# Kernel tuning notes

Hardware: AMD Instinct MI355X
Metric: run time of the kernel (lower is better)

Reference implementation:

```python
import jax, jax.numpy as jnp
import numpy as np

B, L, D, N = 1, 4096, 1536, 12
d = D // N            # head_dim = 128
c = d // 2            # rope channels per head = 64
EPS = 1e-6
MAX_POS = 1024


def setup_inputs() -> dict:
    key = jax.random.key(0)
    ks = jax.random.split(key, 8)
    s = 0.02
    # RoPE tables: freqs[m, j] = m * theta^{-j/c}; torch stores exp(i*ang) as complex64
    inv = 1.0 / (10000.0 ** (jnp.arange(c, dtype=jnp.float32) / c))
    ang = jnp.arange(MAX_POS, dtype=jnp.float32)[:, None] * inv[None, :]
    return {
        'x': jax.random.normal(ks[0], (B, L, D), jnp.float32),
        'seq_lens': jnp.array([L], jnp.int32),
        'grid_sizes': jnp.array([[4, 32, 32]], jnp.int32),  # f*h*w == L
        'freqs_cos': jnp.cos(ang),
        'freqs_sin': jnp.sin(ang),
        'Wq': jax.random.normal(ks[1], (D, D), jnp.float32) * s,
        'bq': jnp.zeros((D,), jnp.float32),
        'Wk': jax.random.normal(ks[2], (D, D), jnp.float32) * s,
        'bk': jnp.zeros((D,), jnp.float32),
        'Wv': jax.random.normal(ks[3], (D, D), jnp.float32) * s,
        'bv': jnp.zeros((D,), jnp.float32),
        'Wo': jax.random.normal(ks[4], (D, D), jnp.float32) * s,
        'bo': jnp.zeros((D,), jnp.float32),
        'gq': jnp.ones((D,), jnp.float32),
        'gk': jnp.ones((D,), jnp.float32),
    }


def rms_norm(x, g):
    # WanRMSNorm over the full model dim, computed in fp32
    v = jnp.mean(x.astype(jnp.float32) ** 2, axis=-1, keepdims=True)
    return (x * jax.lax.rsqrt(v + EPS)).astype(x.dtype) * g


def rope_apply(x4, grid_sizes, fcos, fsin):
    # x4: [B, L, N, d]; grid_sizes: [B, 3]; applies 3D (f,h,w) RoPE per batch
    gs = np.asarray(grid_sizes)  # concrete grid sizes (structural constants)
    c1 = c - 2 * (c // 3)
    c2 = c // 3
    outs = []
    for i in range(x4.shape[0]):
        f, h, w = (int(gs[i, 0]), int(gs[i, 1]), int(gs[i, 2]))
        sl = f * h * w

        def grid(tab):
            a = jnp.broadcast_to(tab[:f, None, None, :c1], (f, h, w, c1))
            b = jnp.broadcast_to(tab[None, :h, None, c1:c1 + c2], (f, h, w, c2))
            cc = jnp.broadcast_to(tab[None, None, :w, c1 + c2:c], (f, h, w, c2))
            return jnp.concatenate([a, b, cc], axis=-1).reshape(sl, 1, c)

        cos_i, sin_i = grid(fcos), grid(fsin)
        xi = x4[i, :sl]                    # [sl, N, d]
        xr, xim = xi[..., 0::2], xi[..., 1::2]  # complex pairs are interleaved
        o_re = xr * cos_i - xim * sin_i
        o_im = xr * sin_i + xim * cos_i
        rot = jnp.stack([o_re, o_im], axis=-1).reshape(sl, x4.shape[2], d)
        outs.append(jnp.concatenate([rot, x4[i, sl:]], axis=0))
    return jnp.stack(outs).astype(x4.dtype)


def reference(x, seq_lens, grid_sizes, freqs_cos, freqs_sin,
              Wq, bq, Wk, bk, Wv, bv, Wo, bo, gq, gk):
    q = rms_norm(x @ Wq.T + bq, gq).reshape(B, L, N, d)
    k = rms_norm(x @ Wk.T + bk, gk).reshape(B, L, N, d)
    v = (x @ Wv.T + bv).reshape(B, L, N, d)
    q = rope_apply(q, grid_sizes, freqs_cos, freqs_sin)
    k = rope_apply(k, grid_sizes, freqs_cos, freqs_sin)
    scale = 1.0 / jnp.sqrt(jnp.float32(d))
    scores = jnp.einsum('bqnd,bknd->bnqk', q, k) * scale
    kmask = jnp.arange(L)[None, :] < seq_lens[:, None]        # [B, L]
    scores = jnp.where(kmask[:, None, None, :], scores, jnp.float32(-1e30))
    p = jax.nn.softmax(scores, axis=-1)
    out = jnp.einsum('bnqk,bknd->bqnd', p, v).reshape(B, L, D)
    return out @ Wo.T + bo
```

## Files before the change

### kernel.cpp

```cpp
#include <hip/hip_runtime.h>

#define L_ 4096
#define D_ 1536
#define NH 12
#define HD 128

typedef __attribute__((ext_vector_type(8))) __bf16 bf16x8;
typedef __attribute__((ext_vector_type(8))) unsigned short ushort8v;
typedef __attribute__((ext_vector_type(4))) float floatx4;

#if __has_builtin(__builtin_amdgcn_exp2f)
#define EXP2F(x) __builtin_amdgcn_exp2f(x)
#else
#define EXP2F(x) exp2f(x)
#endif

__device__ __forceinline__ unsigned short f2bf(float f) {
  union { float f; unsigned int u; } v; v.f = f;
  unsigned int u = v.u;
  return (unsigned short)((u + 0x7fffu + ((u >> 16) & 1u)) >> 16);
}
__device__ __forceinline__ float bf2f(unsigned short h) {
  union { unsigned int u; float f; } v; v.u = ((unsigned int)h) << 16;
  return v.f;
}

__global__ __launch_bounds__(256) void cvt_f32_bf16(const float* __restrict__ in,
                                                    unsigned short* __restrict__ out,
                                                    int n8) {
  int i = blockIdx.x * 256 + threadIdx.x;
  if (i >= n8) return;
  const float4* p = (const float4*)(in + (size_t)i * 8);
  float4 a = p[0], b = p[1];
  ushort8v o;
  o[0] = f2bf(a.x); o[1] = f2bf(a.y); o[2] = f2bf(a.z); o[3] = f2bf(a.w);
  o[4] = f2bf(b.x); o[5] = f2bf(b.y); o[6] = f2bf(b.z); o[7] = f2bf(b.w);
  *(ushort8v*)(out + (size_t)i * 8) = o;
}

template <int MODE>
__device__ __forceinline__ void gemm_core(const unsigned short* __restrict__ A,
                                          const unsigned short* __restrict__ Bw,
                                          const float* __restrict__ bias,
                                          void* __restrict__ Cout,
                                          int M, int Nn, int K,
                                          int m0, int n0,
                                          unsigned short* As, unsigned short* Bs) {
  int t = threadIdx.x;
  int lane = t & 63, wv = t >> 6;
  int wm = (wv & 1) * 64, wn = (wv >> 1) * 64;
  floatx4 zero = {0.f, 0.f, 0.f, 0.f};
  floatx4 acc[4][4];
#pragma unroll
  for (int i = 0; i < 4; ++i)
#pragma unroll
    for (int j = 0; j < 4; ++j) acc[i][j] = zero;
  int fm = lane & 15, fk = (lane >> 4) * 8;

  for (int kt = 0; kt < K; kt += 32) {
    __syncthreads();
#pragma unroll
    for (int it = 0; it < 2; ++it) {
      int c = it * 256 + t;
      int row = c >> 2, col = (c & 3) * 8;
      const unsigned short* ga = A + (size_t)(m0 + row) * K + kt + col;
      const unsigned short* gb = Bw + (size_t)(n0 + row) * K + kt + col;
      __builtin_amdgcn_global_load_lds(
          (const __attribute__((address_space(1))) void*)ga,
          (__attribute__((address_space(3))) void*)((char*)As + (it * 256 + wv * 64) * 16),
          16, 0, 0);
      __builtin_amdgcn_global_load_lds(
          (const __attribute__((address_space(1))) void*)gb,
          (__attribute__((address_space(3))) void*)((char*)Bs + (it * 256 + wv * 64) * 16),
          16, 0, 0);
    }
    __syncthreads();
    bf16x8 af[4], bfr[4];
#pragma unroll
    for (int i = 0; i < 4; ++i) {
      af[i]  = *(const bf16x8*)&As[(wm + 16 * i + fm) * 32 + fk];
      bfr[i] = *(const bf16x8*)&Bs[(wn + 16 * i + fm) * 32 + fk];
    }
#pragma unroll
    for (int i = 0; i < 4; ++i)
#pragma unroll
      for (int j = 0; j < 4; ++j)
        acc[i][j] = __builtin_amdgcn_mfma_f32_16x16x32_bf16(af[i], bfr[j], acc[i][j], 0, 0, 0);
  }

  int fr = (lane >> 4) * 4;
#pragma unroll
  for (int j = 0; j < 4; ++j) {
    int col = n0 + wn + 16 * j + fm;
    float bz = bias[col];
#pragma unroll
    for (int i = 0; i < 4; ++i) {
      int row0 = m0 + wm + 16 * i + fr;
      if (MODE == 2) {
        ushort4 pk = make_ushort4(f2bf(acc[i][j][0] + bz), f2bf(acc[i][j][1] + bz),
                                  f2bf(acc[i][j][2] + bz), f2bf(acc[i][j][3] + bz));
        size_t off = (size_t)(row0 >> 5) * Nn * 32 + (size_t)col * 32 + (row0 & 31);
        *(ushort4*)&((unsigned short*)Cout)[off] = pk;
      } else {
#pragma unroll
        for (int r = 0; r < 4; ++r) {
          float val = acc[i][j][r] + bz;
          if (MODE == 1) ((unsigned short*)Cout)[(size_t)(row0 + r) * Nn + col] = f2bf(val);
          else           ((float*)Cout)[(size_t)(row0 + r) * Nn + col] = val;
        }
      }
    }
  }
}

template <int MODE>
__global__ __launch_bounds__(256) void gemm_bt(const unsigned short* __restrict__ A,
                                               const unsigned short* __restrict__ Bw,
                                               const float* __restrict__ bias,
                                               void* __restrict__ Cout,
                                               int M, int Nn, int K) {
  __shared__ unsigned short As[128 * 32];
  __shared__ unsigned short Bs[128 * 32];
  gemm_core<MODE>(A, Bw, bias, Cout, M, Nn, K, blockIdx.y * 128, blockIdx.x * 128, As, Bs);
}

__global__ __launch_bounds__(256) void gemm_qkv(const unsigned short* __restrict__ xb,
                                                const unsigned short* __restrict__ wq,
                                                const unsigned short* __restrict__ wk,
                                                const unsigned short* __restrict__ wv,
                                                const float* __restrict__ bq,
                                                const float* __restrict__ bk,
                                                const float* __restrict__ bv,
                                                unsigned short* __restrict__ outq,
                                                unsigned short* __restrict__ outk,
                                                unsigned short* __restrict__ outv) {
  __shared__ unsigned short As[128 * 32];
  __shared__ unsigned short Bs[128 * 32];
  int which = blockIdx.x / (D_ / 128);
  int n0 = (blockIdx.x % (D_ / 128)) * 128;
  int m0 = blockIdx.y * 128;
  if (which == 0)
    gemm_core<1>(xb, wq, bq, outq, L_, D_, D_, m0, n0, As, Bs);
  else if (which == 1)
    gemm_core<1>(xb, wk, bk, outk, L_, D_, D_, m0, n0, As, Bs);
  else
    gemm_core<2>(xb, wv, bv, outv, L_, D_, D_, m0, n0, As, Bs);
}

__global__ __launch_bounds__(256) void rmsrope(unsigned short* __restrict__ qb,
                                               unsigned short* __restrict__ kb,
                                               const float* __restrict__ gq,
                                               const float* __restrict__ gk,
                                               const float* __restrict__ fcos,
                                               const float* __restrict__ fsin,
                                               const int* __restrict__ grid_sizes) {
  int row = blockIdx.x;
  unsigned short* buf = (blockIdx.y == 0) ? qb : kb;
  const float* g = (blockIdx.y == 0) ? gq : gk;
  float osc = (blockIdx.y == 0) ? 0.1275174475f : 1.0f;
  int t = threadIdx.x;
  float xr[3], xi[3];
#pragma unroll
  for (int i = 0; i < 3; ++i) {
    int p = t + i * 256;
    unsigned int raw = *(const unsigned int*)&buf[(size_t)row * D_ + 2 * p];
    xr[i] = bf2f((unsigned short)(raw & 0xffffu));
    xi[i] = bf2f((unsigned short)(raw >> 16));
  }
  float ss = 0.f;
#pragma unroll
  for (int i = 0; i < 3; ++i) ss += xr[i] * xr[i] + xi[i] * xi[i];
  for (int off = 32; off > 0; off >>= 1) ss += __shfl_down(ss, off);
  __shared__ float red[4];
  if ((t & 63) == 0) red[t >> 6] = ss;
  __syncthreads();
  float rs = rsqrtf((red[0] + red[1] + red[2] + red[3]) * (1.0f / D_) + 1e-6f);

  int gf = grid_sizes[0], gh = grid_sizes[1], gw = grid_sizes[2];
  int sl = gf * gh * gw;
  int hw = gh * gw;
  int fi = row / hw, rem = row - fi * hw;
  int hi = rem / gw, wi = rem - hi * gw;
  bool dorope = row < sl;
#pragma unroll
  for (int i = 0; i < 3; ++i) {
    int p = t + i * 256;
    int j = p & 63;
    float a = xr[i] * rs * g[2 * p];
    float b = xi[i] * rs * g[2 * p + 1];
    if (dorope) {
      int pos = (j < 22) ? fi : ((j < 43) ? hi : wi);
      float cs = fcos[pos * 64 + j], sn = fsin[pos * 64 + j];
      float oa = a * cs - b * sn;
      float ob = a * sn + b * cs;
      a = oa; b = ob;
    }
    a *= osc; b *= osc;
    unsigned int packed = (unsigned int)f2bf(a) | ((unsigned int)f2bf(b) << 16);
    *(unsigned int*)&buf[(size_t)row * D_ + 2 * p] = packed;
  }
}

__global__ __launch_bounds__(256, 2) void attn5(const unsigned short* __restrict__ Qb,
                                                const unsigned short* __restrict__ Kb,
                                                const unsigned short* __restrict__ Vt,
                                                unsigned short* __restrict__ Ob,
                                                const int* __restrict__ seq_lens) {
  __shared__ unsigned short Ks[2][4096];
  __shared__ unsigned short Vs[2][4096];
  int t = threadIdx.x, lane = t & 63, w = t >> 6;
  int id = blockIdx.x;
  int u = (id & 7) * 48 + (id >> 3);
  int h = u >> 5, qt = u & 31;
  int q0 = qt * 128 + w * 32;
  int seqlen = seq_lens[0];
  int fl = lane & 15, fg = lane >> 4;

  bf16x8 qf[2][4];
#pragma unroll
  for (int nj = 0; nj < 2; ++nj)
#pragma unroll
    for (int kd = 0; kd < 4; ++kd)
      qf[nj][kd] = *(const bf16x8*)&Qb[((size_t)(q0 + nj * 16 + fl) * NH + h) * HD + kd * 32 + fg * 8];

  const unsigned short* kp[2];
  const unsigned short* vp[2];
#pragma unroll
  for (int i = 0; i < 2; ++i) {
    int c = t + i * 256;
    int dgroup = c >> 5, permrow = c & 31;
    int kd = dgroup >> 2, fgc = dgroup & 3, mi = permrow >> 4, flc = permrow & 15;
    int key = (((flc & 12) << 1) | (flc & 3)) + (mi << 2);
    kp[i] = Kb + ((size_t)key * NH + h) * HD + kd * 32 + fgc * 8;
    int vd = c >> 2, vkg = c & 3;
    vp[i] = Vt + ((size_t)(h * HD + vd)) * 32 + vkg * 8;
  }
  const int STEP = 32 * NH * HD;

  auto stage = [&](int b) {
#pragma unroll
    for (int i = 0; i < 2; ++i) {
      __builtin_amdgcn_global_load_lds(
          (const __attribute__((address_space(1))) void*)kp[i],
          (__attribute__((address_space(3))) void*)&Ks[b][(i * 256 + w * 64) * 8],
          16, 0, 0);
      __builtin_amdgcn_global_load_lds(
          (const __attribute__((address_space(1))) void*)vp[i],
          (__attribute__((address_space(3))) void*)&Vs[b][(i * 256 + w * 64) * 8],
          16, 0, 0);
      kp[i] += STEP; vp[i] += STEP;
    }
  };

  floatx4 o[2][8];
  floatx4 zero = {0.f, 0.f, 0.f, 0.f};
#pragma unroll
  for (int nj = 0; nj < 2; ++nj)
#pragma unroll
    for (int nt = 0; nt < 8; ++nt) o[nj][nt] = zero;
  float lr[2] = {0.f, 0.f};

  stage(0);
  for (int kt = 0; kt < L_; kt += 32) {
    int cur = (kt >> 5) & 1;
    __syncthreads();
    if (kt + 32 < L_) stage(cur ^ 1);

    floatx4 s[2][2];
    s[0][0] = zero; s[0][1] = zero; s[1][0] = zero; s[1][1] = zero;
#pragma unroll
    for (int kd = 0; kd < 4; ++kd)
#pragma unroll
      for (int mi = 0; mi < 2; ++mi) {
        bf16x8 kf = *(const bf16x8*)&Ks[cur][(((kd << 2) | fg) * 32 + (mi << 4) + fl) * 8];
#pragma unroll
        for (int nj = 0; nj < 2; ++nj)
          s[mi][nj] = __builtin_amdgcn_mfma_f32_16x16x32_bf16(kf, qf[nj][kd], s[mi][nj], 0, 0, 0);
      }

    bf16x8 pb[2];
    bool full = (kt + 32 <= seqlen);
#pragma unroll
    for (int nj = 0; nj < 2; ++nj) {
      float p[8];
      if (full) {
#pragma unroll
        for (int mi = 0; mi < 2; ++mi)
#pragma unroll
          for (int r = 0; r < 4; ++r) p[mi * 4 + r] = EXP2F(s[mi][nj][r]);
      } else {
#pragma unroll
        for (int mi = 0; mi < 2; ++mi)
#pragma unroll
          for (int r = 0; r < 4; ++r) {
            int key = kt + fg * 8 + mi * 4 + r;
            p[mi * 4 + r] = (key < seqlen) ? EXP2F(s[mi][nj][r]) : 0.f;
          }
      }
      float sum = ((p[0] + p[1]) + (p[2] + p[3])) + ((p[4] + p[5]) + (p[6] + p[7]));
      sum += __shfl_xor(sum, 16);
      sum += __shfl_xor(sum, 32);
      lr[nj] += sum;
      union { unsigned int u[4]; bf16x8 v; } pk;
#pragma unroll
      for (int jj = 0; jj < 4; ++jj) {
        unsigned int a = __builtin_bit_cast(unsigned int, p[2 * jj]) + 0x8000u;
        unsigned int b = __builtin_bit_cast(unsigned int, p[2 * jj + 1]) + 0x8000u;
        pk.u[jj] = (a >> 16) | (b & 0xffff0000u);
      }
      pb[nj] = pk.v;
    }

#pragma unroll
    for (int nt = 0; nt < 8; ++nt) {
      bf16x8 vf = *(const bf16x8*)&Vs[cur][((((nt << 4) + fl) << 2) + fg) * 8];
#pragma unroll
      for (int nj = 0; nj < 2; ++nj)
        o[nj][nt] = __builtin_amdgcn_mfma_f32_16x16x32_bf16(pb[nj], vf, o[nj][nt], 0, 0, 0);
    }
  }

#pragma unroll
  for (int nj = 0; nj < 2; ++nj) {
    float inv = 1.0f / lr[nj];
    float i0 = __shfl(inv, fg * 4 + 0);
    float i1 = __shfl(inv, fg * 4 + 1);
    float i2 = __shfl(inv, fg * 4 + 2);
    float i3 = __shfl(inv, fg * 4 + 3);
    int rowb = q0 + nj * 16 + fg * 4;
#pragma unroll
    for (int nt = 0; nt < 8; ++nt) {
      int dcol = h * HD + nt * 16 + fl;
      Ob[(size_t)(rowb + 0) * D_ + dcol] = f2bf(o[nj][nt][0] * i0);
      Ob[(size_t)(rowb + 1) * D_ + dcol] = f2bf(o[nj][nt][1] * i1);
      Ob[(size_t)(rowb + 2) * D_ + dcol] = f2bf(o[nj][nt][2] * i2);
      Ob[(size_t)(rowb + 3) * D_ + dcol] = f2bf(o[nj][nt][3] * i3);
    }
  }
}

extern "C" void kernel_launch(void* const* d_in, const int* in_sizes, int n_in,
                              void* d_out, int out_size, void* d_ws, size_t ws_size,
                              hipStream_t stream) {
  (void)in_sizes; (void)n_in; (void)out_size;
  const float* x    = (const float*)d_in[0];
  const int* seqln  = (const int*)d_in[1];
  const int* gsz    = (const int*)d_in[2];
  const float* fcos = (const float*)d_in[3];
  const float* fsin = (const float*)d_in[4];
  const float* Wq = (const float*)d_in[5];
  const float* bq = (const float*)d_in[6];
  const float* Wk = (const float*)d_in[7];
  const float* bk = (const float*)d_in[8];
  const float* Wv = (const float*)d_in[9];
  const float* bv = (const float*)d_in[10];
  const float* Wo = (const float*)d_in[11];
  const float* bo = (const float*)d_in[12];
  const float* gq = (const float*)d_in[13];
  const float* gk = (const float*)d_in[14];

  char* ws = (char*)d_ws;
  size_t LD2 = (size_t)L_ * D_ * 2;
  size_t WD2 = (size_t)D_ * D_ * 2;
  unsigned short* xb  = (unsigned short*)(ws);
  unsigned short* qb  = (unsigned short*)(ws + LD2);
  unsigned short* kb  = (unsigned short*)(ws + 2 * LD2);
  unsigned short* vtb = (unsigned short*)(ws + 3 * LD2);
  unsigned short* wb0 = (unsigned short*)(ws + 4 * LD2);
  unsigned short* ab  = xb;

  int nx8 = L_ * D_ / 8, nw8 = D_ * D_ / 8;
  dim3 gg(D_ / 128, L_ / 128);

  cvt_f32_bf16<<<(nx8 + 255) / 256, 256, 0, stream>>>(x, xb, nx8);

  if (ws_size >= 4 * LD2 + 3 * WD2) {
    unsigned short* wb1 = (unsigned short*)(ws + 4 * LD2 + WD2);
    unsigned short* wb2 = (unsigned short*)(ws + 4 * LD2 + 2 * WD2);
    cvt_f32_bf16<<<(nw8 + 255) / 256, 256, 0, stream>>>(Wq, wb0, nw8);
    cvt_f32_bf16<<<(nw8 + 255) / 256, 256, 0, stream>>>(Wk, wb1, nw8);
    cvt_f32_bf16<<<(nw8 + 255) / 256, 256, 0, stream>>>(Wv, wb2, nw8);
    gemm_qkv<<<dim3(3 * D_ / 128, L_ / 128), 256, 0, stream>>>(
        xb, wb0, wb1, wb2, bq, bk, bv, qb, kb, vtb);
  } else {
    cvt_f32_bf16<<<(nw8 + 255) / 256, 256, 0, stream>>>(Wq, wb0, nw8);
    gemm_bt<1><<<gg, 256, 0, stream>>>(xb, wb0, bq, qb, L_, D_, D_);
    cvt_f32_bf16<<<(nw8 + 255) / 256, 256, 0, stream>>>(Wk, wb0, nw8);
    gemm_bt<1><<<gg, 256, 0, stream>>>(xb, wb0, bk, kb, L_, D_, D_);
    cvt_f32_bf16<<<(nw8 + 255) / 256, 256, 0, stream>>>(Wv, wb0, nw8);
    gemm_bt<2><<<gg, 256, 0, stream>>>(xb, wb0, bv, vtb, L_, D_, D_);
  }

  rmsrope<<<dim3(L_, 2), 256, 0, stream>>>(qb, kb, gq, gk, fcos, fsin, gsz);

  attn5<<<dim3(384), 256, 0, stream>>>(qb, kb, vtb, ab, seqln);

  cvt_f32_bf16<<<(nw8 + 255) / 256, 256, 0, stream>>>(Wo, wb0, nw8);
  gemm_bt<0><<<gg, 256, 0, stream>>>(ab, wb0, bo, d_out, L_, D_, D_);
}
```

Baseline: 465.6 us.

## Split attention key range across two wave groups and merge partial outputs

The attention kernel now launches 512 threads per block in two groups of four waves. Each group processes half of the key sequence (2048 keys) for the same 128 queries, using its own double-buffered K/V LDS tiles. At the end, group 1 writes its partial outputs and row sums to shared memory and group 0 adds them before normalizing and storing. The aim is to double parallelism per block, since 384 blocks underfill the GPU, and to shorten the serial key loop. The costs are more LDS per block and an extra reduction step through shared memory. The V tile layout is also reindexed.

```diff
diff --git a/kernel.cpp b/kernel.cpp
--- a/kernel.cpp
+++ b/kernel.cpp
@@ -201,18 +201,22 @@
   }
 }
 
-__global__ __launch_bounds__(256, 2) void attn5(const unsigned short* __restrict__ Qb,
+__global__ __launch_bounds__(512, 4) void attn6(const unsigned short* __restrict__ Qb,
                                                 const unsigned short* __restrict__ Kb,
                                                 const unsigned short* __restrict__ Vt,
                                                 unsigned short* __restrict__ Ob,
                                                 const int* __restrict__ seq_lens) {
-  __shared__ unsigned short Ks[2][4096];
-  __shared__ unsigned short Vs[2][4096];
+  __shared__ char smem[66048];
   int t = threadIdx.x, lane = t & 63, w = t >> 6;
+  int g = w >> 2, p = w & 3, tg = t & 255;
+  unsigned short* Ksg = (unsigned short*)(smem + g * 32768);
+  unsigned short* Vsg = (unsigned short*)(smem + g * 32768 + 16384);
+  float* lbuf = (float*)(smem + 65536);
+
   int id = blockIdx.x;
   int u = (id & 7) * 48 + (id >> 3);
   int h = u >> 5, qt = u & 31;
-  int q0 = qt * 128 + w * 32;
+  int q0 = qt * 128 + p * 32;
   int seqlen = seq_lens[0];
   int fl = lane & 15, fg = lane >> 4;
 
@@ -227,13 +231,13 @@
   const unsigned short* vp[2];
 #pragma unroll
   for (int i = 0; i < 2; ++i) {
-    int c = t + i * 256;
+    int c = tg + i * 256;
     int dgroup = c >> 5, permrow = c & 31;
     int kd = dgroup >> 2, fgc = dgroup & 3, mi = permrow >> 4, flc = permrow & 15;
     int key = (((flc & 12) << 1) | (flc & 3)) + (mi << 2);
-    kp[i] = Kb + ((size_t)key * NH + h) * HD + kd * 32 + fgc * 8;
-    int vd = c >> 2, vkg = c & 3;
-    vp[i] = Vt + ((size_t)(h * HD + vd)) * 32 + vkg * 8;
+    kp[i] = Kb + ((size_t)(g * 2048 + key) * NH + h) * HD + kd * 32 + fgc * 8;
+    int vd = c & 127, vkg = c >> 7;
+    vp[i] = Vt + (size_t)(g * 64) * (D_ * 32) + ((size_t)(h * HD + vd)) * 32 + vkg * 8;
   }
   const int STEP = 32 * NH * HD;
 
@@ -242,11 +246,11 @@
     for (int i = 0; i < 2; ++i) {
       __builtin_amdgcn_global_load_lds(
           (const __attribute__((address_space(1))) void*)kp[i],
-          (__attribute__((address_space(3))) void*)&Ks[b][(i * 256 + w * 64) * 8],
+          (__attribute__((address_space(3))) void*)&Ksg[b * 4096 + (i * 256 + p * 64) * 8],
           16, 0, 0);
       __builtin_amdgcn_global_load_lds(
           (const __attribute__((address_space(1))) void*)vp[i],
-          (__attribute__((address_space(3))) void*)&Vs[b][(i * 256 + w * 64) * 8],
+          (__attribute__((address_space(3))) void*)&Vsg[b * 4096 + (i * 256 + p * 64) * 8],
           16, 0, 0);
       kp[i] += STEP; vp[i] += STEP;
     }
@@ -261,10 +265,10 @@
   float lr[2] = {0.f, 0.f};
 
   stage(0);
-  for (int kt = 0; kt < L_; kt += 32) {
+  for (int kt = 0; kt < 2048; kt += 32) {
     int cur = (kt >> 5) & 1;
     __syncthreads();
-    if (kt + 32 < L_) stage(cur ^ 1);
+    if (kt + 32 < 2048) stage(cur ^ 1);
 
     floatx4 s[2][2];
     s[0][0] = zero; s[0][1] = zero; s[1][0] = zero; s[1][1] = zero;
@@ -272,40 +276,37 @@
     for (int kd = 0; kd < 4; ++kd)
 #pragma unroll
       for (int mi = 0; mi < 2; ++mi) {
-        bf16x8 kf = *(const bf16x8*)&Ks[cur][(((kd << 2) | fg) * 32 + (mi << 4) + fl) * 8];
+        bf16x8 kf = *(const bf16x8*)&Ksg[cur * 4096 + (((kd << 2) | fg) * 32 + (mi << 4) + fl) * 8];
 #pragma unroll
         for (int nj = 0; nj < 2; ++nj)
           s[mi][nj] = __builtin_amdgcn_mfma_f32_16x16x32_bf16(kf, qf[nj][kd], s[mi][nj], 0, 0, 0);
       }
 
     bf16x8 pb[2];
-    bool full = (kt + 32 <= seqlen);
+    bool full = (g * 2048 + kt + 32 <= seqlen);
 #pragma unroll
     for (int nj = 0; nj < 2; ++nj) {
-      float p[8];
+      float pv[8];
       if (full) {
 #pragma unroll
         for (int mi = 0; mi < 2; ++mi)
 #pragma unroll
-          for (int r = 0; r < 4; ++r) p[mi * 4 + r] = EXP2F(s[mi][nj][r]);
+          for (int r = 0; r < 4; ++r) pv[mi * 4 + r] = EXP2F(s[mi][nj][r]);
       } else {
 #pragma unroll
         for (int mi = 0; mi < 2; ++mi)
 #pragma unroll
           for (int r = 0; r < 4; ++r) {
-            int key = kt + fg * 8 + mi * 4 + r;
-            p[mi * 4 + r] = (key < seqlen) ? EXP2F(s[mi][nj][r]) : 0.f;
+            int key = g * 2048 + kt + fg * 8 + mi * 4 + r;
+            pv[mi * 4 + r] = (key < seqlen) ? EXP2F(s[mi][nj][r]) : 0.f;
           }
       }
-      float sum = ((p[0] + p[1]) + (p[2] + p[3])) + ((p[4] + p[5]) + (p[6] + p[7]));
-      sum += __shfl_xor(sum, 16);
-      sum += __shfl_xor(sum, 32);
-      lr[nj] += sum;
+      lr[nj] += ((pv[0] + pv[1]) + (pv[2] + pv[3])) + ((pv[4] + pv[5]) + (pv[6] + pv[7]));
       union { unsigned int u[4]; bf16x8 v; } pk;
 #pragma unroll
       for (int jj = 0; jj < 4; ++jj) {
-        unsigned int a = __builtin_bit_cast(unsigned int, p[2 * jj]) + 0x8000u;
-        unsigned int b = __builtin_bit_cast(unsigned int, p[2 * jj + 1]) + 0x8000u;
+        unsigned int a = __builtin_bit_cast(unsigned int, pv[2 * jj]) + 0x8000u;
+        unsigned int b = __builtin_bit_cast(unsigned int, pv[2 * jj + 1]) + 0x8000u;
         pk.u[jj] = (a >> 16) | (b & 0xffff0000u);
       }
       pb[nj] = pk.v;
@@ -313,7 +314,7 @@
 
 #pragma unroll
     for (int nt = 0; nt < 8; ++nt) {
-      bf16x8 vf = *(const bf16x8*)&Vs[cur][((((nt << 4) + fl) << 2) + fg) * 8];
+      bf16x8 vf = *(const bf16x8*)&Vsg[cur * 4096 + ((fg << 7) + (nt << 4) + fl) * 8];
 #pragma unroll
       for (int nj = 0; nj < 2; ++nj)
         o[nj][nt] = __builtin_amdgcn_mfma_f32_16x16x32_bf16(pb[nj], vf, o[nj][nt], 0, 0, 0);
@@ -322,19 +323,53 @@
 
 #pragma unroll
   for (int nj = 0; nj < 2; ++nj) {
-    float inv = 1.0f / lr[nj];
-    float i0 = __shfl(inv, fg * 4 + 0);
-    float i1 = __shfl(inv, fg * 4 + 1);
-    float i2 = __shfl(inv, fg * 4 + 2);
-    float i3 = __shfl(inv, fg * 4 + 3);
-    int rowb = q0 + nj * 16 + fg * 4;
-#pragma unroll
-    for (int nt = 0; nt < 8; ++nt) {
-      int dcol = h * HD + nt * 16 + fl;
-      Ob[(size_t)(rowb + 0) * D_ + dcol] = f2bf(o[nj][nt][0] * i0);
-      Ob[(size_t)(rowb + 1) * D_ + dcol] = f2bf(o[nj][nt][1] * i1);
-      Ob[(size_t)(rowb + 2) * D_ + dcol] = f2bf(o[nj][nt][2] * i2);
-      Ob[(size_t)(rowb + 3) * D_ + dcol] = f2bf(o[nj][nt][3] * i3);
+    lr[nj] += __shfl_xor(lr[nj], 16);
+    lr[nj] += __shfl_xor(lr[nj], 32);
+  }
+
+  __syncthreads();
+  float* cb = (float*)smem;
+  if (g == 1) {
+    float* dst = cb + p * 4096 + lane * 64;
+#pragma unroll
+    for (int nj = 0; nj < 2; ++nj)
+#pragma unroll
+      for (int nt = 0; nt < 8; ++nt) ((floatx4*)dst)[nj * 8 + nt] = o[nj][nt];
+    if (fg == 0) {
+#pragma unroll
+      for (int nj = 0; nj < 2; ++nj) lbuf[p * 32 + nj * 16 + fl] = lr[nj];
+    }
+  }
+  __syncthreads();
+  if (g == 0) {
+    float* src = cb + p * 4096 + lane * 64;
+#pragma unroll
+    for (int nj = 0; nj < 2; ++nj) {
+#pragma unroll
+      for (int nt = 0; nt < 8; ++nt) {
+        floatx4 add = ((floatx4*)src)[nj * 8 + nt];
+        o[nj][nt][0] += add[0]; o[nj][nt][1] += add[1];
+        o[nj][nt][2] += add[2]; o[nj][nt][3] += add[3];
+      }
+      lr[nj] += lbuf[p * 32 + nj * 16 + fl];
+    }
+
+#pragma unroll
+    for (int nj = 0; nj < 2; ++nj) {
+      float inv = 1.0f / lr[nj];
+      float i0 = __shfl(inv, fg * 4 + 0);
+      float i1 = __shfl(inv, fg * 4 + 1);
+      float i2 = __shfl(inv, fg * 4 + 2);
+      float i3 = __shfl(inv, fg * 4 + 3);
+      int rowb = q0 + nj * 16 + fg * 4;
+#pragma unroll
+      for (int nt = 0; nt < 8; ++nt) {
+        int dcol = h * HD + nt * 16 + fl;
+        Ob[(size_t)(rowb + 0) * D_ + dcol] = f2bf(o[nj][nt][0] * i0);
+        Ob[(size_t)(rowb + 1) * D_ + dcol] = f2bf(o[nj][nt][1] * i1);
+        Ob[(size_t)(rowb + 2) * D_ + dcol] = f2bf(o[nj][nt][2] * i2);
+        Ob[(size_t)(rowb + 3) * D_ + dcol] = f2bf(o[nj][nt][3] * i3);
+      }
     }
   }
 }
@@ -393,7 +428,7 @@
 
   rmsrope<<<dim3(L_, 2), 256, 0, stream>>>(qb, kb, gq, gk, fcos, fsin, gsz);
 
-  attn5<<<dim3(384), 256, 0, stream>>>(qb, kb, vtb, ab, seqln);
+  attn6<<<dim3(384), 512, 0, stream>>>(qb, kb, vtb, ab, seqln);
 
   cvt_f32_bf16<<<(nw8 + 255) / 256, 256, 0, stream>>>(Wo, wb0, nw8);
   gemm_bt<0><<<gg, 256, 0, stream>>>(ab, wb0, bo, d_out, L_, D_, D_);
```

Result: slower. 550.5 us (+18.2%).

## Split attention over two KV halves with fp32 partials and combine kernel

Applied to the files above, without the earlier changes.

Adds a split-KV attention kernel that launches 768 blocks, each covering half of the key range, and writes unnormalized fp32 partial outputs and row sums. A separate combine kernel then adds the two halves and normalizes into bf16. This raises block count for better CU occupancy at the cost of extra fp32 global traffic and one more launch. It also moves the row-sum shuffle reduction out of the inner loop and changes the V LDS staging layout in the existing kernel too. The partial softmax is valid only because no max subtraction is used.

```diff
diff --git a/kernel.cpp b/kernel.cpp
--- a/kernel.cpp
+++ b/kernel.cpp
@@ -201,6 +201,167 @@
   }
 }
 
+__global__ __launch_bounds__(256, 2) void attn7(const unsigned short* __restrict__ Qb,
+                                                const unsigned short* __restrict__ Kb,
+                                                const unsigned short* __restrict__ Vt,
+                                                float* __restrict__ Op0,
+                                                float* __restrict__ Op1,
+                                                float* __restrict__ lp,
+                                                const int* __restrict__ seq_lens) {
+  __shared__ unsigned short Ks[2][4096];
+  __shared__ unsigned short Vs[2][4096];
+  int t = threadIdx.x, lane = t & 63, w = t >> 6;
+  int id = blockIdx.x;
+  int u2 = (id & 7) * 96 + (id >> 3);
+  int half = u2 & 1, v = u2 >> 1;
+  int h = v >> 5, qt = v & 31;
+  int q0 = qt * 128 + w * 32;
+  int kv0 = half * 2048;
+  float* Opart = half ? Op1 : Op0;
+  float* lpart = lp + (size_t)half * L_ * NH;
+  int seqlen = seq_lens[0];
+  int fl = lane & 15, fg = lane >> 4;
+
+  bf16x8 qf[2][4];
+#pragma unroll
+  for (int nj = 0; nj < 2; ++nj)
+#pragma unroll
+    for (int kd = 0; kd < 4; ++kd)
+      qf[nj][kd] = *(const bf16x8*)&Qb[((size_t)(q0 + nj * 16 + fl) * NH + h) * HD + kd * 32 + fg * 8];
+
+  const unsigned short* kp[2];
+  const unsigned short* vp[2];
+#pragma unroll
+  for (int i = 0; i < 2; ++i) {
+    int c = t + i * 256;
+    int dgroup = c >> 5, permrow = c & 31;
+    int kd = dgroup >> 2, fgc = dgroup & 3, mi = permrow >> 4, flc = permrow & 15;
+    int key = (((flc & 12) << 1) | (flc & 3)) + (mi << 2);
+    kp[i] = Kb + ((size_t)(kv0 + key) * NH + h) * HD + kd * 32 + fgc * 8;
+    int vd = c & 127, vkg = c >> 7;
+    vp[i] = Vt + (size_t)(kv0 >> 5) * (D_ * 32) + ((size_t)(h * HD + vd)) * 32 + vkg * 8;
+  }
+  const int STEP = 32 * NH * HD;
+
+  auto stage = [&](int b) {
+#pragma unroll
+    for (int i = 0; i < 2; ++i) {
+      __builtin_amdgcn_global_load_lds(
+          (const __attribute__((address_space(1))) void*)kp[i],
+          (__attribute__((address_space(3))) void*)&Ks[b][(i * 256 + w * 64) * 8],
+          16, 0, 0);
+      __builtin_amdgcn_global_load_lds(
+          (const __attribute__((address_space(1))) void*)vp[i],
+          (__attribute__((address_space(3))) void*)&Vs[b][(i * 256 + w * 64) * 8],
+          16, 0, 0);
+      kp[i] += STEP; vp[i] += STEP;
+    }
+  };
+
+  floatx4 o[2][8];
+  floatx4 zero = {0.f, 0.f, 0.f, 0.f};
+#pragma unroll
+  for (int nj = 0; nj < 2; ++nj)
+#pragma unroll
+    for (int nt = 0; nt < 8; ++nt) o[nj][nt] = zero;
+  float lr[2] = {0.f, 0.f};
+
+  stage(0);
+  for (int kt = 0; kt < 2048; kt += 32) {
+    int cur = (kt >> 5) & 1;
+    __syncthreads();
+    if (kt + 32 < 2048) stage(cur ^ 1);
+
+    floatx4 s[2][2];
+    s[0][0] = zero; s[0][1] = zero; s[1][0] = zero; s[1][1] = zero;
+#pragma unroll
+    for (int kd = 0; kd < 4; ++kd)
+#pragma unroll
+      for (int mi = 0; mi < 2; ++mi) {
+        bf16x8 kf = *(const bf16x8*)&Ks[cur][(((kd << 2) | fg) * 32 + (mi << 4) + fl) * 8];
+#pragma unroll
+        for (int nj = 0; nj < 2; ++nj)
+          s[mi][nj] = __builtin_amdgcn_mfma_f32_16x16x32_bf16(kf, qf[nj][kd], s[mi][nj], 0, 0, 0);
+      }
+
+    bf16x8 pb[2];
+    bool full = (kv0 + kt + 32 <= seqlen);
+#pragma unroll
+    for (int nj = 0; nj < 2; ++nj) {
+      float pv[8];
+      if (full) {
+#pragma unroll
+        for (int mi = 0; mi < 2; ++mi)
+#pragma unroll
+          for (int r = 0; r < 4; ++r) pv[mi * 4 + r] = EXP2F(s[mi][nj][r]);
+      } else {
+#pragma unroll
+        for (int mi = 0; mi < 2; ++mi)
+#pragma unroll
+          for (int r = 0; r < 4; ++r) {
+            int key = kv0 + kt + fg * 8 + mi * 4 + r;
+            pv[mi * 4 + r] = (key < seqlen) ? EXP2F(s[mi][nj][r]) : 0.f;
+          }
+      }
+      lr[nj] += ((pv[0] + pv[1]) + (pv[2] + pv[3])) + ((pv[4] + pv[5]) + (pv[6] + pv[7]));
+      union { unsigned int u[4]; bf16x8 v; } pk;
+#pragma unroll
+      for (int jj = 0; jj < 4; ++jj) {
+        unsigned int a = __builtin_bit_cast(unsigned int, pv[2 * jj]) + 0x8000u;
+        unsigned int b = __builtin_bit_cast(unsigned int, pv[2 * jj + 1]) + 0x8000u;
+        pk.u[jj] = (a >> 16) | (b & 0xffff0000u);
+      }
+      pb[nj] = pk.v;
+    }
+
+#pragma unroll
+    for (int nt = 0; nt < 8; ++nt) {
+      bf16x8 vf = *(const bf16x8*)&Vs[cur][((fg << 7) + (nt << 4) + fl) * 8];
+#pragma unroll
+      for (int nj = 0; nj < 2; ++nj)
+        o[nj][nt] = __builtin_amdgcn_mfma_f32_16x16x32_bf16(pb[nj], vf, o[nj][nt], 0, 0, 0);
+    }
+  }
+
+#pragma unroll
+  for (int nj = 0; nj < 2; ++nj) {
+    lr[nj] += __shfl_xor(lr[nj], 16);
+    lr[nj] += __shfl_xor(lr[nj], 32);
+    int rowb = q0 + nj * 16 + fg * 4;
+#pragma unroll
+    for (int nt = 0; nt < 8; ++nt) {
+      int dcol = h * HD + nt * 16 + fl;
+      Opart[(size_t)(rowb + 0) * D_ + dcol] = o[nj][nt][0];
+      Opart[(size_t)(rowb + 1) * D_ + dcol] = o[nj][nt][1];
+      Opart[(size_t)(rowb + 2) * D_ + dcol] = o[nj][nt][2];
+      Opart[(size_t)(rowb + 3) * D_ + dcol] = o[nj][nt][3];
+    }
+    if (fg == 0) lpart[(size_t)(q0 + nj * 16 + fl) * NH + h] = lr[nj];
+  }
+}
+
+__global__ __launch_bounds__(256) void attn_combine(const float* __restrict__ Op0,
+                                                    const float* __restrict__ Op1,
+                                                    const float* __restrict__ lp,
+                                                    unsigned short* __restrict__ out) {
+  int gid = blockIdx.x * 256 + threadIdx.x;
+  int q = gid / (D_ / 8);
+  int col = (gid - q * (D_ / 8)) * 8;
+  int h = col >> 7;
+  float l0 = lp[(size_t)q * NH + h];
+  float l1 = lp[(size_t)L_ * NH + (size_t)q * NH + h];
+  float inv = 1.0f / (l0 + l1);
+  const float4* p0 = (const float4*)(Op0 + (size_t)q * D_ + col);
+  const float4* p1 = (const float4*)(Op1 + (size_t)q * D_ + col);
+  float4 a0 = p0[0], a1 = p0[1], b0 = p1[0], b1 = p1[1];
+  ushort8v o;
+  o[0] = f2bf((a0.x + b0.x) * inv); o[1] = f2bf((a0.y + b0.y) * inv);
+  o[2] = f2bf((a0.z + b0.z) * inv); o[3] = f2bf((a0.w + b0.w) * inv);
+  o[4] = f2bf((a1.x + b1.x) * inv); o[5] = f2bf((a1.y + b1.y) * inv);
+  o[6] = f2bf((a1.z + b1.z) * inv); o[7] = f2bf((a1.w + b1.w) * inv);
+  *(ushort8v*)(out + (size_t)q * D_ + col) = o;
+}
+
 __global__ __launch_bounds__(256, 2) void attn5(const unsigned short* __restrict__ Qb,
                                                 const unsigned short* __restrict__ Kb,
                                                 const unsigned short* __restrict__ Vt,
@@ -232,7 +393,7 @@
     int kd = dgroup >> 2, fgc = dgroup & 3, mi = permrow >> 4, flc = permrow & 15;
     int key = (((flc & 12) << 1) | (flc & 3)) + (mi << 2);
     kp[i] = Kb + ((size_t)key * NH + h) * HD + kd * 32 + fgc * 8;
-    int vd = c >> 2, vkg = c & 3;
+    int vd = c & 127, vkg = c >> 7;
     vp[i] = Vt + ((size_t)(h * HD + vd)) * 32 + vkg * 8;
   }
   const int STEP = 32 * NH * HD;
@@ -282,30 +443,27 @@
     bool full = (kt + 32 <= seqlen);
 #pragma unroll
     for (int nj = 0; nj < 2; ++nj) {
-      float p[8];
+      float pv[8];
       if (full) {
 #pragma unroll
         for (int mi = 0; mi < 2; ++mi)
 #pragma unroll
-          for (int r = 0; r < 4; ++r) p[mi * 4 + r] = EXP2F(s[mi][nj][r]);
+          for (int r = 0; r < 4; ++r) pv[mi * 4 + r] = EXP2F(s[mi][nj][r]);
       } else {
 #pragma unroll
         for (int mi = 0; mi < 2; ++mi)
 #pragma unroll
           for (int r = 0; r < 4; ++r) {
             int key = kt + fg * 8 + mi * 4 + r;
-            p[mi * 4 + r] = (key < seqlen) ? EXP2F(s[mi][nj][r]) : 0.f;
+            pv[mi * 4 + r] = (key < seqlen) ? EXP2F(s[mi][nj][r]) : 0.f;
           }
       }
-      float sum = ((p[0] + p[1]) + (p[2] + p[3])) + ((p[4] + p[5]) + (p[6] + p[7]));
-      sum += __shfl_xor(sum, 16);
-      sum += __shfl_xor(sum, 32);
-      lr[nj] += sum;
+      lr[nj] += ((pv[0] + pv[1]) + (pv[2] + pv[3])) + ((pv[4] + pv[5]) + (pv[6] + pv[7]));
       union { unsigned int u[4]; bf16x8 v; } pk;
 #pragma unroll
       for (int jj = 0; jj < 4; ++jj) {
-        unsigned int a = __builtin_bit_cast(unsigned int, p[2 * jj]) + 0x8000u;
-        unsigned int b = __builtin_bit_cast(unsigned int, p[2 * jj + 1]) + 0x8000u;
+        unsigned int a = __builtin_bit_cast(unsigned int, pv[2 * jj]) + 0x8000u;
+        unsigned int b = __builtin_bit_cast(unsigned int, pv[2 * jj + 1]) + 0x8000u;
         pk.u[jj] = (a >> 16) | (b & 0xffff0000u);
       }
       pb[nj] = pk.v;
@@ -313,7 +471,7 @@
 
 #pragma unroll
     for (int nt = 0; nt < 8; ++nt) {
-      bf16x8 vf = *(const bf16x8*)&Vs[cur][((((nt << 4) + fl) << 2) + fg) * 8];
+      bf16x8 vf = *(const bf16x8*)&Vs[cur][((fg << 7) + (nt << 4) + fl) * 8];
 #pragma unroll
       for (int nj = 0; nj < 2; ++nj)
         o[nj][nt] = __builtin_amdgcn_mfma_f32_16x16x32_bf16(pb[nj], vf, o[nj][nt], 0, 0, 0);
@@ -322,19 +480,17 @@
 
 #pragma unroll
   for (int nj = 0; nj < 2; ++nj) {
+    lr[nj] += __shfl_xor(lr[nj], 16);
+    lr[nj] += __shfl_xor(lr[nj], 32);
     float inv = 1.0f / lr[nj];
-    float i0 = __shfl(inv, fg * 4 + 0);
-    float i1 = __shfl(inv, fg * 4 + 1);
-    float i2 = __shfl(inv, fg * 4 + 2);
-    float i3 = __shfl(inv, fg * 4 + 3);
     int rowb = q0 + nj * 16 + fg * 4;
 #pragma unroll
     for (int nt = 0; nt < 8; ++nt) {
       int dcol = h * HD + nt * 16 + fl;
-      Ob[(size_t)(rowb + 0) * D_ + dcol] = f2bf(o[nj][nt][0] * i0);
-      Ob[(size_t)(rowb + 1) * D_ + dcol] = f2bf(o[nj][nt][1] * i1);
-      Ob[(size_t)(rowb + 2) * D_ + dcol] = f2bf(o[nj][nt][2] * i2);
-      Ob[(size_t)(rowb + 3) * D_ + dcol] = f2bf(o[nj][nt][3] * i3);
+      Ob[(size_t)(rowb + 0) * D_ + dcol] = f2bf(o[nj][nt][0] * inv);
+      Ob[(size_t)(rowb + 1) * D_ + dcol] = f2bf(o[nj][nt][1] * inv);
+      Ob[(size_t)(rowb + 2) * D_ + dcol] = f2bf(o[nj][nt][2] * inv);
+      Ob[(size_t)(rowb + 3) * D_ + dcol] = f2bf(o[nj][nt][3] * inv);
     }
   }
 }
@@ -360,8 +516,10 @@
   const float* gk = (const float*)d_in[14];
 
   char* ws = (char*)d_ws;
-  size_t LD2 = (size_t)L_ * D_ * 2;
-  size_t WD2 = (size_t)D_ * D_ * 2;
+  size_t LD2  = (size_t)L_ * D_ * 2;
+  size_t WD2  = (size_t)D_ * D_ * 2;
+  size_t LD4  = (size_t)L_ * D_ * 4;
+  size_t LNH4 = (size_t)L_ * NH * 4;
   unsigned short* xb  = (unsigned short*)(ws);
   unsigned short* qb  = (unsigned short*)(ws + LD2);
   unsigned short* kb  = (unsigned short*)(ws + 2 * LD2);
@@ -374,7 +532,8 @@
 
   cvt_f32_bf16<<<(nx8 + 255) / 256, 256, 0, stream>>>(x, xb, nx8);
 
-  if (ws_size >= 4 * LD2 + 3 * WD2) {
+  bool fusedw = ws_size >= 4 * LD2 + 3 * WD2;
+  if (fusedw) {
     unsigned short* wb1 = (unsigned short*)(ws + 4 * LD2 + WD2);
     unsigned short* wb2 = (unsigned short*)(ws + 4 * LD2 + 2 * WD2);
     cvt_f32_bf16<<<(nw8 + 255) / 256, 256, 0, stream>>>(Wq, wb0, nw8);
@@ -393,7 +552,17 @@
 
   rmsrope<<<dim3(L_, 2), 256, 0, stream>>>(qb, kb, gq, gk, fcos, fsin, gsz);
 
-  attn5<<<dim3(384), 256, 0, stream>>>(qb, kb, vtb, ab, seqln);
+  size_t splitBase = 4 * LD2 + 3 * WD2;
+  bool splitk = fusedw && (ws_size >= splitBase + LD4 + 2 * LNH4);
+  if (splitk) {
+    float* Op0 = (float*)d_out;
+    float* Op1 = (float*)(ws + splitBase);
+    float* lp  = (float*)(ws + splitBase + LD4);
+    attn7<<<dim3(768), 256, 0, stream>>>(qb, kb, vtb, Op0, Op1, lp, seqln);
+    attn_combine<<<dim3(L_ * D_ / 8 / 256), 256, 0, stream>>>(Op0, Op1, lp, ab);
+  } else {
+    attn5<<<dim3(384), 256, 0, stream>>>(qb, kb, vtb, ab, seqln);
+  }
 
   cvt_f32_bf16<<<(nw8 + 255) / 256, 256, 0, stream>>>(Wo, wb0, nw8);
   gemm_bt<0><<<gg, 256, 0, stream>>>(ab, wb0, bo, d_out, L_, D_, D_);
```

After: 404.8 us. 13.1% less time.
